# Optimization experiments

Measured on AMD Instinct MI355X. Metric: run time of the kernel, lower is better.

The kernel has to match this reference:

```python
import jax, jax.numpy as jnp
import numpy as np

B, S, H, L = 8, 512, 768, 8192


def setup_inputs() -> dict:
    key = jax.random.key(0)
    k1, k2, k3, k4 = jax.random.split(key, 4)
    inputs = jax.random.normal(k1, (B, S, H), dtype=jnp.float32)
    masks = jax.random.randint(k2, (B, 1, S), 0, 2).astype(jnp.bool_)
    # guarantee at least one valid position per row so softmax is finite
    masks = masks.at[:, :, 0].set(True)
    # xavier-normal label embedding [L, H] (frozen param in original)
    std_emb = float(np.sqrt(2.0 / (L + H)))
    label_embedding = jax.random.normal(k3, (L, H), dtype=jnp.float32) * std_emb
    # xavier-uniform key weight [H, H] (nn.Linear stores W as [out, in])
    lim = float(np.sqrt(6.0 / (H + H)))
    W_key = jax.random.uniform(k4, (H, H), dtype=jnp.float32, minval=-lim, maxval=lim)
    return {"inputs": inputs, "masks": masks, "label_embedding": label_embedding, "W_key": W_key}


def reference(inputs, masks, label_embedding, W_key):
    # key projection: inputs @ W_key^T  -> [B, S, H]
    attn_key = jnp.einsum("bsh,kh->bsk", inputs, W_key)
    # scores: label_emb @ key^T -> [B, L, S] (no 1/sqrt(d) scaling, per original)
    scores = jnp.einsum("lh,bsh->bls", label_embedding, attn_key)
    scores = jnp.where(masks, scores, -jnp.inf)  # masks [B,1,S] broadcasts over L
    attn = jax.nn.softmax(scores, axis=-1)
    # weighted sum of raw inputs -> [B, L, H]
    return jnp.einsum("bls,bsh->blh", attn, inputs)
```

## Files before the change

kernel.cpp:

```cpp
#include <hip/hip_runtime.h>
#include <hip/hip_bf16.h>
#include <math.h>

#define NB 8
#define NS 512
#define NH 768
#define NL 8192

typedef __attribute__((ext_vector_type(8))) __bf16 bf16x8;
typedef __attribute__((ext_vector_type(4))) float f32x4;

static __device__ __forceinline__ f32x4 mfma_bf16(bf16x8 a, bf16x8 b, f32x4 c) {
  return __builtin_amdgcn_mfma_f32_16x16x32_bf16(a, b, c, 0, 0, 0);
}

static __device__ __forceinline__ void llds16(const void* g, void* l) {
  __builtin_amdgcn_global_load_lds(
      (const __attribute__((address_space(1))) unsigned int*)g,
      (__attribute__((address_space(3))) unsigned int*)l, 16, 0, 0);
}

static __device__ __forceinline__ bf16x8 load_cvt8(const float* __restrict__ p) {
  f32x4 u0 = *(const f32x4*)p;
  f32x4 u1 = *(const f32x4*)(p + 4);
  bf16x8 r;
  r[0] = (__bf16)u0[0]; r[1] = (__bf16)u0[1]; r[2] = (__bf16)u0[2]; r[3] = (__bf16)u0[3];
  r[4] = (__bf16)u1[0]; r[5] = (__bf16)u1[1]; r[6] = (__bf16)u1[2]; r[7] = (__bf16)u1[3];
  return r;
}

__global__ void mask_kernel(const unsigned char* __restrict__ m,
                            float* __restrict__ mbias) {
  __shared__ int s_i8, s_f32;
  if (threadIdx.x == 0) { s_i8 = 0; s_f32 = 0; }
  __syncthreads();
  const unsigned int* md = (const unsigned int*)m;
  int li8 = 0, lf = 0;
  for (int i = threadIdx.x; i < 1024; i += blockDim.x) {
    unsigned int d = md[i];
    if (d == 0x3F800000u) lf = 1;
    if (d & 0xFFFFFF00u) li8 = 1;
  }
  if (li8) atomicOr(&s_i8, 1);
  if (lf) atomicOr(&s_f32, 1);
  __syncthreads();
  int f = s_f32 ? 2 : (s_i8 ? 1 : 0);
  for (int i = threadIdx.x; i < NB * NS; i += blockDim.x) {
    int v;
    if (f == 1)      v = (((const unsigned char*)m)[i] != 0);
    else if (f == 2) v = (((const float*)m)[i] != 0.0f);
    else             v = (((const int*)m)[i] != 0);
    mbias[i] = v ? 0.0f : -INFINITY;
  }
}

#define XT8 393216
#define WT8 466944
#define ET8 1253376
__global__ __launch_bounds__(256) void cast_all_kernel(
    const float* __restrict__ X, const float* __restrict__ W,
    const float* __restrict__ E, __bf16* __restrict__ dstbase) {
  size_t t8 = (size_t)blockIdx.x * 256 + threadIdx.x;
  const float* src;
  size_t off;
  if (t8 < XT8)      { src = X; off = t8 * 8; }
  else if (t8 < WT8) { src = W; off = (t8 - XT8) * 8; }
  else               { src = E; off = (t8 - WT8) * 8; }
  bf16x8 v = load_cvt8(src + off);
  *(bf16x8*)(dstbase + t8 * 8) = v;
}

__global__ __launch_bounds__(256) void transpose_kernel(const float* __restrict__ X,
                                                        __bf16* __restrict__ XT) {
  __shared__ float t[64][65];
  const int b = blockIdx.z, s0 = blockIdx.y * 64, h0 = blockIdx.x * 64;
  const int j = threadIdx.x & 63, i0 = threadIdx.x >> 6;
#pragma unroll
  for (int i = i0; i < 64; i += 4) t[i][j] = X[((size_t)b * NS + s0 + i) * NH + h0 + j];
  __syncthreads();
  __bf16* XTb = XT + ((size_t)b * NH + h0) * NS + s0;
  const int si = threadIdx.x & 63, j0 = threadIdx.x >> 6;
#pragma unroll
  for (int jj = j0; jj < 64; jj += 4)
    XTb[(size_t)jj * NS + si] = (__bf16)t[si][jj];
}

__global__ __launch_bounds__(256, 4) void proj64_kernel(
    const __bf16* __restrict__ Xbf, const __bf16* __restrict__ Wbf,
    __bf16* __restrict__ Kout) {
  const int tid = threadIdx.x, lane = tid & 63, wid = tid >> 6;
  const int c = lane & 15, g = lane >> 4;
  const int wm = wid >> 1, wn = wid & 1;
  const int m0 = blockIdx.x * 64, n0 = blockIdx.y * 64;
  __shared__ __align__(16) unsigned char Ast[2][4096];
  __shared__ __align__(16) unsigned char Bst[2][4096];

  f32x4 acc[2][2];
#pragma unroll
  for (int i = 0; i < 2; ++i)
#pragma unroll
    for (int j = 0; j < 2; ++j) acc[i][j] = (f32x4){0.f, 0.f, 0.f, 0.f};

  auto stage = [&](int buf, int k0) {
    int idx = wid * 64 + lane;
    int row = idx >> 2, slot = idx & 3;
    llds16(Xbf + (size_t)(m0 + row) * NH + k0 + slot * 8, &Ast[buf][wid * 1024]);
    llds16(Wbf + (size_t)(n0 + row) * NH + k0 + slot * 8, &Bst[buf][wid * 1024]);
  };

  stage(0, 0);
  __syncthreads();
  int cur = 0;
  for (int t = 0; t < 24; ++t) {
    if (t < 23) stage(cur ^ 1, (t + 1) * 32);
    bf16x8 af[2], bfr[2];
#pragma unroll
    for (int fm = 0; fm < 2; ++fm)
      af[fm] = *(const bf16x8*)&Ast[cur][(wm * 32 + fm * 16 + c) * 64 + g * 16];
#pragma unroll
    for (int fn = 0; fn < 2; ++fn)
      bfr[fn] = *(const bf16x8*)&Bst[cur][(wn * 32 + fn * 16 + c) * 64 + g * 16];
#pragma unroll
    for (int fm = 0; fm < 2; ++fm)
#pragma unroll
      for (int fn = 0; fn < 2; ++fn)
        acc[fm][fn] = mfma_bf16(af[fm], bfr[fn], acc[fm][fn]);
    __syncthreads();
    cur ^= 1;
  }
#pragma unroll
  for (int fm = 0; fm < 2; ++fm)
#pragma unroll
    for (int r = 0; r < 4; ++r) {
      int row = m0 + wm * 32 + fm * 16 + g * 4 + r;
#pragma unroll
      for (int fn = 0; fn < 2; ++fn)
        Kout[(size_t)row * NH + n0 + wn * 32 + fn * 16 + c] = (__bf16)acc[fm][fn][r];
    }
}

__global__ __launch_bounds__(512, 1) void fused_attn_kernel(
    const __bf16* __restrict__ Ebf,
    const __bf16* __restrict__ Kbf,
    const __bf16* __restrict__ XTbf,
    const float* __restrict__ mbias,
    float* __restrict__ Out) {
  const int tid = threadIdx.x, lane = tid & 63, wid = tid >> 6;
  const int c = lane & 15, g = lane >> 4;
  const int b = blockIdx.y;
  const int R0 = blockIdx.x * 64;

  __shared__ __align__(16) __bf16 Plds[64 * 512];
  __shared__ __align__(16) unsigned char Ast[2][4096];
  __shared__ __align__(16) unsigned char Bst[2][32768];
  __shared__ float red[8][64];

  const __bf16* Kb0 = Kbf + (size_t)b * NS * NH;

  f32x4 acc[4][4];
#pragma unroll
  for (int i = 0; i < 4; ++i)
#pragma unroll
    for (int j = 0; j < 4; ++j) acc[i][j] = (f32x4){0.f, 0.f, 0.f, 0.f};

  auto stage1 = [&](int buf, int k0) {
    if (wid < 4) {
      int idx = wid * 64 + lane;
      int row = idx >> 2, slot = idx & 3;
      llds16(Ebf + (size_t)(R0 + row) * NH + k0 + slot * 8, &Ast[buf][wid * 1024]);
    }
#pragma unroll
    for (int it = 0; it < 4; ++it) {
      int ch = it * 8 + wid;
      int idx = ch * 64 + lane;
      int srow = idx >> 2, slot = idx & 3;
      llds16(Kb0 + (size_t)srow * NH + k0 + slot * 8, &Bst[buf][ch * 1024]);
    }
  };

  stage1(0, 0);
  __syncthreads();
  int cur = 0;
  for (int t = 0; t < 24; ++t) {
    if (t < 23) stage1(cur ^ 1, (t + 1) * 32);
    bf16x8 af[4], bfr[4];
#pragma unroll
    for (int fm = 0; fm < 4; ++fm)
      af[fm] = *(const bf16x8*)&Ast[cur][(fm * 16 + c) * 64 + g * 16];
#pragma unroll
    for (int fn = 0; fn < 4; ++fn)
      bfr[fn] = *(const bf16x8*)&Bst[cur][(wid * 64 + fn * 16 + c) * 64 + g * 16];
#pragma unroll
    for (int fm = 0; fm < 4; ++fm)
#pragma unroll
      for (int fn = 0; fn < 4; ++fn)
        acc[fm][fn] = mfma_bf16(af[fm], bfr[fn], acc[fm][fn]);
    __syncthreads();
    cur ^= 1;
  }

  float bias[4];
#pragma unroll
  for (int fn = 0; fn < 4; ++fn) bias[fn] = mbias[b * NS + wid * 64 + fn * 16 + c];

#pragma unroll
  for (int fm = 0; fm < 4; ++fm)
#pragma unroll
    for (int r = 0; r < 4; ++r) {
      float v = -INFINITY;
#pragma unroll
      for (int fn = 0; fn < 4; ++fn) v = fmaxf(v, acc[fm][fn][r] + bias[fn]);
      v = fmaxf(v, __shfl_xor(v, 1));
      v = fmaxf(v, __shfl_xor(v, 2));
      v = fmaxf(v, __shfl_xor(v, 4));
      v = fmaxf(v, __shfl_xor(v, 8));
      if (c == 0) red[wid][fm * 16 + g * 4 + r] = v;
    }
  __syncthreads();
  float rmax[4][4];
#pragma unroll
  for (int fm = 0; fm < 4; ++fm)
#pragma unroll
    for (int r = 0; r < 4; ++r) {
      int l = fm * 16 + g * 4 + r;
      float v = red[0][l];
#pragma unroll
      for (int w = 1; w < 8; ++w) v = fmaxf(v, red[w][l]);
      rmax[fm][r] = v;
    }
  __syncthreads();

#pragma unroll
  for (int fm = 0; fm < 4; ++fm)
#pragma unroll
    for (int r = 0; r < 4; ++r) {
      float s = 0.f;
#pragma unroll
      for (int fn = 0; fn < 4; ++fn) {
        float p = __expf(acc[fm][fn][r] + bias[fn] - rmax[fm][r]);
        acc[fm][fn][r] = p;
        s += p;
      }
      s += __shfl_xor(s, 1);
      s += __shfl_xor(s, 2);
      s += __shfl_xor(s, 4);
      s += __shfl_xor(s, 8);
      if (c == 0) red[wid][fm * 16 + g * 4 + r] = s;
    }
  __syncthreads();

#pragma unroll
  for (int fm = 0; fm < 4; ++fm)
#pragma unroll
    for (int r = 0; r < 4; ++r) {
      int l = fm * 16 + g * 4 + r;
      float s = red[0][l];
#pragma unroll
      for (int w = 1; w < 8; ++w) s += red[w][l];
      float inv = 1.0f / s;
#pragma unroll
      for (int fn = 0; fn < 4; ++fn) {
        int col = wid * 64 + fn * 16 + c;
        Plds[l * 512 + (col ^ ((l & 7) << 3))] = (__bf16)(acc[fm][fn][r] * inv);
      }
    }
  __syncthreads();

  const __bf16* XTb0 = XTbf + (size_t)b * NH * NS;
  float* Ob = Out + ((size_t)b * NL + R0) * NH;

  for (int nh = 0; nh < 2; ++nh) {
    const int h0 = nh * 384;
    f32x4 acc2[4][3];
#pragma unroll
    for (int i = 0; i < 4; ++i)
#pragma unroll
      for (int j = 0; j < 3; ++j) acc2[i][j] = (f32x4){0.f, 0.f, 0.f, 0.f};

    auto stage2 = [&](int buf, int ks) {
#pragma unroll
      for (int j = 0; j < 3; ++j) {
        int ch = wid * 3 + j;
        int idx = ch * 64 + lane;
        int hrow = idx >> 2, slot = idx & 3;
        llds16(XTb0 + (size_t)(h0 + hrow) * NS + ks + slot * 8, &Bst[buf][ch * 1024]);
      }
    };

    stage2(0, 0);
    __syncthreads();
    cur = 0;
    for (int t = 0; t < 16; ++t) {
      if (t < 15) stage2(cur ^ 1, (t + 1) * 32);
      int kk = t * 32 + g * 8;
      bf16x8 af[4], bfr[3];
#pragma unroll
      for (int fm = 0; fm < 4; ++fm) {
        int l = fm * 16 + c;
        af[fm] = *(const bf16x8*)&Plds[l * 512 + (kk ^ ((l & 7) << 3))];
      }
#pragma unroll
      for (int fn = 0; fn < 3; ++fn)
        bfr[fn] = *(const bf16x8*)&Bst[cur][(wid * 48 + fn * 16 + c) * 64 + g * 16];
#pragma unroll
      for (int fm = 0; fm < 4; ++fm)
#pragma unroll
        for (int fn = 0; fn < 3; ++fn)
          acc2[fm][fn] = mfma_bf16(af[fm], bfr[fn], acc2[fm][fn]);
      __syncthreads();
      cur ^= 1;
    }
#pragma unroll
    for (int fm = 0; fm < 4; ++fm)
#pragma unroll
      for (int r = 0; r < 4; ++r) {
        int l = fm * 16 + g * 4 + r;
#pragma unroll
        for (int fn = 0; fn < 3; ++fn) {
          int h = h0 + wid * 48 + fn * 16 + c;
          Ob[(size_t)l * NH + h] = acc2[fm][fn][r];
        }
      }
  }
}

__global__ void detect_mask_kernel(const unsigned char* __restrict__ m,
                                   int* __restrict__ flag) {
  __shared__ int s_i8, s_f32;
  if (threadIdx.x == 0) { s_i8 = 0; s_f32 = 0; }
  __syncthreads();
  const unsigned int* md = (const unsigned int*)m;
  int li8 = 0, lf = 0;
  for (int i = threadIdx.x; i < 1024; i += blockDim.x) {
    unsigned int d = md[i];
    if (d == 0x3F800000u) lf = 1;
    if (d & 0xFFFFFF00u) li8 = 1;
  }
  if (li8) atomicOr(&s_i8, 1);
  if (lf) atomicOr(&s_f32, 1);
  __syncthreads();
  if (threadIdx.x == 0) *flag = s_f32 ? 2 : (s_i8 ? 1 : 0);
}

__global__ void expand_mask_kernel(const void* __restrict__ m,
                                   const int* __restrict__ flag,
                                   float* __restrict__ mbias) {
  int i = blockIdx.x * blockDim.x + threadIdx.x;
  int f = *flag;
  int v;
  if (f == 1)      v = (((const unsigned char*)m)[i] != 0);
  else if (f == 2) v = (((const float*)m)[i] != 0.0f);
  else             v = (((const int*)m)[i] != 0);
  mbias[i] = v ? 0.0f : -INFINITY;
}

__global__ __launch_bounds__(256) void cast_kernel(const float* __restrict__ src,
                                                   __bf16* __restrict__ dst) {
  size_t idx = ((size_t)blockIdx.x * 256 + threadIdx.x) * 8;
  bf16x8 v = load_cvt8(src + idx);
  *(bf16x8*)(dst + idx) = v;
}

__global__ __launch_bounds__(256) void proj_kernel(const float* __restrict__ X,
                                                   const float* __restrict__ W,
                                                   __bf16* __restrict__ Kout) {
  const int tid = threadIdx.x;
  const int lane = tid & 63, wid = tid >> 6;
  const int c = lane & 15, g = lane >> 4;
  const int wm = wid >> 1, wn = wid & 1;
  const int m0 = blockIdx.x * 64 + wm * 32;
  const int n0 = blockIdx.y * 64 + wn * 32;
  f32x4 acc[2][2] = {};
  const float* Xp = X + (size_t)(m0 + c) * NH + g * 8;
  const float* Wp = W + (size_t)(n0 + c) * NH + g * 8;
  for (int k = 0; k < NH; k += 32) {
    bf16x8 a0 = load_cvt8(Xp + k);
    bf16x8 a1 = load_cvt8(Xp + 16 * NH + k);
    bf16x8 b0 = load_cvt8(Wp + k);
    bf16x8 b1 = load_cvt8(Wp + 16 * NH + k);
    acc[0][0] = mfma_bf16(a0, b0, acc[0][0]);
    acc[0][1] = mfma_bf16(a0, b1, acc[0][1]);
    acc[1][0] = mfma_bf16(a1, b0, acc[1][0]);
    acc[1][1] = mfma_bf16(a1, b1, acc[1][1]);
  }
#pragma unroll
  for (int fm = 0; fm < 2; ++fm)
#pragma unroll
    for (int fn = 0; fn < 2; ++fn)
#pragma unroll
      for (int r = 0; r < 4; ++r) {
        int row = m0 + fm * 16 + g * 4 + r;
        int col = n0 + fn * 16 + c;
        Kout[(size_t)row * NH + col] = (__bf16)acc[fm][fn][r];
      }
}

__global__ __launch_bounds__(512) void label_attn_kernel(
    const __bf16* __restrict__ Ebf, const __bf16* __restrict__ Kbf,
    const __bf16* __restrict__ XTbf, const float* __restrict__ mbias,
    float* __restrict__ Out) {
  const int tid = threadIdx.x;
  const int lane = tid & 63, wid = tid >> 6;
  const int c = lane & 15, g = lane >> 4;
  const int wm = wid >> 2, wn = wid & 3;
  const int b = blockIdx.y;
  const int R0 = blockIdx.x * 64;
  __shared__ alignas(16) __bf16 Plds[64 * 512];
  __shared__ float redM[4][64];
  __shared__ float redS[4][64];
  f32x4 acc[2][8];
#pragma unroll
  for (int i = 0; i < 2; ++i)
#pragma unroll
    for (int j = 0; j < 8; ++j) acc[i][j] = (f32x4){0.f, 0.f, 0.f, 0.f};
  const __bf16* Ea = Ebf + (size_t)(R0 + wm * 32 + c) * NH + g * 8;
  const __bf16* Kb = Kbf + ((size_t)b * NS + wn * 128 + c) * NH + g * 8;
  float bias[8];
#pragma unroll
  for (int fn = 0; fn < 8; ++fn) bias[fn] = mbias[b * NS + wn * 128 + fn * 16 + c];
  for (int k = 0; k < NH; k += 32) {
    bf16x8 a0 = *(const bf16x8*)(Ea + k);
    bf16x8 a1 = *(const bf16x8*)(Ea + 16 * NH + k);
#pragma unroll
    for (int fn = 0; fn < 8; ++fn) {
      bf16x8 bb = *(const bf16x8*)(Kb + (size_t)fn * 16 * NH + k);
      acc[0][fn] = mfma_bf16(a0, bb, acc[0][fn]);
      acc[1][fn] = mfma_bf16(a1, bb, acc[1][fn]);
    }
  }
  float pmax[2][4];
#pragma unroll
  for (int fm = 0; fm < 2; ++fm)
#pragma unroll
    for (int r = 0; r < 4; ++r) {
      float v = -INFINITY;
#pragma unroll
      for (int fn = 0; fn < 8; ++fn) v = fmaxf(v, acc[fm][fn][r] + bias[fn]);
#pragma unroll
      for (int off = 1; off < 16; off <<= 1) v = fmaxf(v, __shfl_xor(v, off));
      pmax[fm][r] = v;
    }
  if (c == 0) {
#pragma unroll
    for (int fm = 0; fm < 2; ++fm)
#pragma unroll
      for (int r = 0; r < 4; ++r)
        redM[wn][wm * 32 + fm * 16 + g * 4 + r] = pmax[fm][r];
  }
  __syncthreads();
  float rmax[2][4];
#pragma unroll
  for (int fm = 0; fm < 2; ++fm)
#pragma unroll
    for (int r = 0; r < 4; ++r) {
      int row = wm * 32 + fm * 16 + g * 4 + r;
      rmax[fm][r] = fmaxf(fmaxf(redM[0][row], redM[1][row]),
                          fmaxf(redM[2][row], redM[3][row]));
    }
  float psum[2][4] = {{0.f, 0.f, 0.f, 0.f}, {0.f, 0.f, 0.f, 0.f}};
#pragma unroll
  for (int fm = 0; fm < 2; ++fm)
#pragma unroll
    for (int fn = 0; fn < 8; ++fn) {
      int col = wn * 128 + fn * 16 + c;
#pragma unroll
      for (int r = 0; r < 4; ++r) {
        int row = wm * 32 + fm * 16 + g * 4 + r;
        float p = __expf(acc[fm][fn][r] + bias[fn] - rmax[fm][r]);
        psum[fm][r] += p;
        Plds[row * 512 + (col ^ ((row & 7) << 3))] = (__bf16)p;
      }
    }
#pragma unroll
  for (int fm = 0; fm < 2; ++fm)
#pragma unroll
    for (int r = 0; r < 4; ++r) {
      float v = psum[fm][r];
#pragma unroll
      for (int off = 1; off < 16; off <<= 1) v += __shfl_xor(v, off);
      psum[fm][r] = v;
    }
  if (c == 0) {
#pragma unroll
    for (int fm = 0; fm < 2; ++fm)
#pragma unroll
      for (int r = 0; r < 4; ++r)
        redS[wn][wm * 32 + fm * 16 + g * 4 + r] = psum[fm][r];
  }
  __syncthreads();
  float inv[2][4];
#pragma unroll
  for (int fm = 0; fm < 2; ++fm)
#pragma unroll
    for (int r = 0; r < 4; ++r) {
      int row = wm * 32 + fm * 16 + g * 4 + r;
      float s = redS[0][row] + redS[1][row] + redS[2][row] + redS[3][row];
      inv[fm][r] = 1.0f / s;
    }
  f32x4 acc2[2][12];
#pragma unroll
  for (int i = 0; i < 2; ++i)
#pragma unroll
    for (int j = 0; j < 12; ++j) acc2[i][j] = (f32x4){0.f, 0.f, 0.f, 0.f};
  const __bf16* XTb = XTbf + ((size_t)b * NH + wn * 192 + c) * NS + g * 8;
  const int r0 = wm * 32 + c;
  const int r1 = r0 + 16;
  for (int ks = 0; ks < NS; ks += 32) {
    int kk = ks + g * 8;
    bf16x8 a0 = *(const bf16x8*)&Plds[r0 * 512 + (kk ^ ((r0 & 7) << 3))];
    bf16x8 a1 = *(const bf16x8*)&Plds[r1 * 512 + (kk ^ ((r1 & 7) << 3))];
#pragma unroll
    for (int fn = 0; fn < 12; ++fn) {
      bf16x8 bb = *(const bf16x8*)(XTb + (size_t)fn * 16 * NS + ks);
      acc2[0][fn] = mfma_bf16(a0, bb, acc2[0][fn]);
      acc2[1][fn] = mfma_bf16(a1, bb, acc2[1][fn]);
    }
  }
  float* Ob = Out + ((size_t)b * NL + R0) * NH;
#pragma unroll
  for (int fm = 0; fm < 2; ++fm)
#pragma unroll
    for (int r = 0; r < 4; ++r) {
      int row = wm * 32 + fm * 16 + g * 4 + r;
      float sc = inv[fm][r];
#pragma unroll
      for (int fn = 0; fn < 12; ++fn) {
        int h = wn * 192 + fn * 16 + c;
        Ob[(size_t)row * NH + h] = acc2[fm][fn][r] * sc;
      }
    }
}

extern "C" void kernel_launch(void* const* d_in, const int* in_sizes, int n_in,
                              void* d_out, int out_size, void* d_ws, size_t ws_size,
                              hipStream_t stream) {
  const float* X = (const float*)d_in[0];
  const void* masks = d_in[1];
  const float* E = (const float*)d_in[2];
  const float* W = (const float*)d_in[3];
  float* Out = (float*)d_out;

  char* ws = (char*)d_ws;
  const size_t NEED = 32653312;

  if (ws_size >= NEED) {
    __bf16* Xbf  = (__bf16*)ws;
    __bf16* Wbf  = (__bf16*)(ws + 6291456);
    __bf16* Ebf  = (__bf16*)(ws + 7471104);
    __bf16* Kbf  = (__bf16*)(ws + 20054016);
    __bf16* XTbf = (__bf16*)(ws + 26345472);
    float* mbias = (float*)(ws + 32636928);

    mask_kernel<<<1, 256, 0, stream>>>((const unsigned char*)masks, mbias);
    cast_all_kernel<<<4896, 256, 0, stream>>>(X, W, E, Xbf);
    transpose_kernel<<<dim3(12, 8, 8), 256, 0, stream>>>(X, XTbf);
    proj64_kernel<<<dim3(64, 12), 256, 0, stream>>>(Xbf, Wbf, Kbf);
    fused_attn_kernel<<<dim3(128, 8), 512, 0, stream>>>(Ebf, Kbf, XTbf, mbias, Out);
  } else {
    __bf16* Kbf  = (__bf16*)ws;
    __bf16* XTbf = (__bf16*)(ws + 6291456);
    __bf16* Ebf  = (__bf16*)(ws + 12582912);
    float* mbias = (float*)(ws + 25165824);
    int* flag    = (int*)(ws + 25182208);

    detect_mask_kernel<<<1, 256, 0, stream>>>((const unsigned char*)masks, flag);
    expand_mask_kernel<<<16, 256, 0, stream>>>(masks, flag, mbias);
    proj_kernel<<<dim3(64, 12), 256, 0, stream>>>(X, W, Kbf);
    transpose_kernel<<<dim3(12, 8, 8), 256, 0, stream>>>(X, XTbf);
    cast_kernel<<<3072, 256, 0, stream>>>(E, Ebf);
    label_attn_kernel<<<dim3(128, 8), 512, 0, stream>>>(Ebf, Kbf, XTbf, mbias, Out);
  }
}
```

Baseline: 474.6 us.

## Split fused attention into scores kernel and separate PV GEMM via workspace

The fused attention kernel is split in two. The first kernel computes scores and softmax and writes the bf16 probabilities P (64 MB) to a workspace buffer. A separate 128x128-tiled pv_kernel then multiplies P by the transposed inputs. Dropping the 64 KB LDS P buffer lets the scores kernel declare higher occupancy, and the PV GEMM gets a better tile shape, at the cost of extra global traffic to write and reread P. The cast and transpose kernels are also merged into a single launch.

```diff
diff --git a/kernel.cpp b/kernel.cpp
--- a/kernel.cpp
+++ b/kernel.cpp
@@ -57,32 +57,37 @@
 #define XT8 393216
 #define WT8 466944
 #define ET8 1253376
-__global__ __launch_bounds__(256) void cast_all_kernel(
+#define CAST_BLOCKS 4896
+__global__ __launch_bounds__(256) void prep_kernel(
     const float* __restrict__ X, const float* __restrict__ W,
-    const float* __restrict__ E, __bf16* __restrict__ dstbase) {
-  size_t t8 = (size_t)blockIdx.x * 256 + threadIdx.x;
-  const float* src;
-  size_t off;
-  if (t8 < XT8)      { src = X; off = t8 * 8; }
-  else if (t8 < WT8) { src = W; off = (t8 - XT8) * 8; }
-  else               { src = E; off = (t8 - WT8) * 8; }
-  bf16x8 v = load_cvt8(src + off);
-  *(bf16x8*)(dstbase + t8 * 8) = v;
-}
-
-__global__ __launch_bounds__(256) void transpose_kernel(const float* __restrict__ X,
-                                                        __bf16* __restrict__ XT) {
+    const float* __restrict__ E, __bf16* __restrict__ dstbase,
+    __bf16* __restrict__ XT) {
   __shared__ float t[64][65];
-  const int b = blockIdx.z, s0 = blockIdx.y * 64, h0 = blockIdx.x * 64;
-  const int j = threadIdx.x & 63, i0 = threadIdx.x >> 6;
-#pragma unroll
-  for (int i = i0; i < 64; i += 4) t[i][j] = X[((size_t)b * NS + s0 + i) * NH + h0 + j];
-  __syncthreads();
-  __bf16* XTb = XT + ((size_t)b * NH + h0) * NS + s0;
-  const int si = threadIdx.x & 63, j0 = threadIdx.x >> 6;
-#pragma unroll
-  for (int jj = j0; jj < 64; jj += 4)
-    XTb[(size_t)jj * NS + si] = (__bf16)t[si][jj];
+  const int bx = blockIdx.x;
+  if (bx < CAST_BLOCKS) {
+    size_t t8 = (size_t)bx * 256 + threadIdx.x;
+    const float* src;
+    size_t off;
+    if (t8 < XT8)      { src = X; off = t8 * 8; }
+    else if (t8 < WT8) { src = W; off = (t8 - XT8) * 8; }
+    else               { src = E; off = (t8 - WT8) * 8; }
+    bf16x8 v = load_cvt8(src + off);
+    *(bf16x8*)(dstbase + t8 * 8) = v;
+  } else {
+    const int tb = bx - CAST_BLOCKS;
+    const int hb = tb % 12, sb = (tb / 12) % 8, b = tb / 96;
+    const int s0 = sb * 64, h0 = hb * 64;
+    const int j = threadIdx.x & 63, i0 = threadIdx.x >> 6;
+#pragma unroll
+    for (int i = i0; i < 64; i += 4)
+      t[i][j] = X[((size_t)b * NS + s0 + i) * NH + h0 + j];
+    __syncthreads();
+    __bf16* XTb = XT + ((size_t)b * NH + h0) * NS + s0;
+    const int si = threadIdx.x & 63, j0 = threadIdx.x >> 6;
+#pragma unroll
+    for (int jj = j0; jj < 64; jj += 4)
+      XTb[(size_t)jj * NS + si] = (__bf16)t[si][jj];
+  }
 }
 
 __global__ __launch_bounds__(256, 4) void proj64_kernel(
@@ -139,18 +144,16 @@
     }
 }
 
-__global__ __launch_bounds__(512, 1) void fused_attn_kernel(
+__global__ __launch_bounds__(512, 4) void scores64_kernel(
     const __bf16* __restrict__ Ebf,
     const __bf16* __restrict__ Kbf,
-    const __bf16* __restrict__ XTbf,
     const float* __restrict__ mbias,
-    float* __restrict__ Out) {
+    __bf16* __restrict__ Pws) {
   const int tid = threadIdx.x, lane = tid & 63, wid = tid >> 6;
   const int c = lane & 15, g = lane >> 4;
   const int b = blockIdx.y;
   const int R0 = blockIdx.x * 64;
 
-  __shared__ __align__(16) __bf16 Plds[64 * 512];
   __shared__ __align__(16) unsigned char Ast[2][4096];
   __shared__ __align__(16) unsigned char Bst[2][32768];
   __shared__ float red[8][64];
@@ -249,6 +252,7 @@
     }
   __syncthreads();
 
+  __bf16* Plin = (__bf16*)Bst;
 #pragma unroll
   for (int fm = 0; fm < 4; ++fm)
 #pragma unroll
@@ -261,67 +265,82 @@
 #pragma unroll
       for (int fn = 0; fn < 4; ++fn) {
         int col = wid * 64 + fn * 16 + c;
-        Plds[l * 512 + (col ^ ((l & 7) << 3))] = (__bf16)(acc[fm][fn][r] * inv);
+        Plin[l * 512 + col] = (__bf16)(acc[fm][fn][r] * inv);
       }
     }
   __syncthreads();
 
-  const __bf16* XTb0 = XTbf + (size_t)b * NH * NS;
-  float* Ob = Out + ((size_t)b * NL + R0) * NH;
-
-  for (int nh = 0; nh < 2; ++nh) {
-    const int h0 = nh * 384;
-    f32x4 acc2[4][3];
-#pragma unroll
-    for (int i = 0; i < 4; ++i)
-#pragma unroll
-      for (int j = 0; j < 3; ++j) acc2[i][j] = (f32x4){0.f, 0.f, 0.f, 0.f};
-
-    auto stage2 = [&](int buf, int ks) {
-#pragma unroll
-      for (int j = 0; j < 3; ++j) {
-        int ch = wid * 3 + j;
-        int idx = ch * 64 + lane;
-        int hrow = idx >> 2, slot = idx & 3;
-        llds16(XTb0 + (size_t)(h0 + hrow) * NS + ks + slot * 8, &Bst[buf][ch * 1024]);
-      }
-    };
-
-    stage2(0, 0);
+  __bf16* Pb = Pws + ((size_t)b * NL + R0) * NS;
+#pragma unroll
+  for (int i = 0; i < 8; ++i) {
+    int row = wid * 8 + i;
+    bf16x8 v = *(const bf16x8*)&Plin[row * 512 + lane * 8];
+    *(bf16x8*)(Pb + (size_t)row * NS + lane * 8) = v;
+  }
+}
+
+__global__ __launch_bounds__(256, 3) void pv_kernel(
+    const __bf16* __restrict__ Pws,
+    const __bf16* __restrict__ XTbf,
+    float* __restrict__ Out) {
+  const int tid = threadIdx.x, lane = tid & 63, wid = tid >> 6;
+  const int c = lane & 15, g = lane >> 4;
+  const int wm = wid >> 1, wn = wid & 1;
+  const int b = blockIdx.z;
+  const size_t rowbase = (size_t)b * NL + (size_t)blockIdx.x * 128;
+  const int h0 = blockIdx.y * 128;
+  __shared__ __align__(16) unsigned char smem[2][16384];
+  const __bf16* Xb0 = XTbf + (size_t)b * NH * NS;
+
+  f32x4 acc[4][4];
+#pragma unroll
+  for (int i = 0; i < 4; ++i)
+#pragma unroll
+    for (int j = 0; j < 4; ++j) acc[i][j] = (f32x4){0.f, 0.f, 0.f, 0.f};
+
+  auto stage = [&](int buf, int k0) {
+#pragma unroll
+    for (int it = 0; it < 2; ++it) {
+      int ch = it * 4 + wid;
+      int idx = ch * 64 + lane;
+      int row = idx >> 2, slot = idx & 3;
+      llds16(Pws + (rowbase + row) * NS + k0 + slot * 8, &smem[buf][ch * 1024]);
+      llds16(Xb0 + (size_t)(h0 + row) * NS + k0 + slot * 8, &smem[buf][8192 + ch * 1024]);
+    }
+  };
+
+  stage(0, 0);
+  __syncthreads();
+  int cur = 0;
+  for (int t = 0; t < 16; ++t) {
+    if (t < 15) stage(cur ^ 1, (t + 1) * 32);
+    const unsigned char* A = smem[cur];
+    const unsigned char* B = smem[cur] + 8192;
+    bf16x8 af[4], bfr[4];
+#pragma unroll
+    for (int fm = 0; fm < 4; ++fm)
+      af[fm] = *(const bf16x8*)(A + (wm * 64 + fm * 16 + c) * 64 + g * 16);
+#pragma unroll
+    for (int fn = 0; fn < 4; ++fn)
+      bfr[fn] = *(const bf16x8*)(B + (wn * 64 + fn * 16 + c) * 64 + g * 16);
+#pragma unroll
+    for (int fm = 0; fm < 4; ++fm)
+#pragma unroll
+      for (int fn = 0; fn < 4; ++fn)
+        acc[fm][fn] = mfma_bf16(af[fm], bfr[fn], acc[fm][fn]);
     __syncthreads();
-    cur = 0;
-    for (int t = 0; t < 16; ++t) {
-      if (t < 15) stage2(cur ^ 1, (t + 1) * 32);
-      int kk = t * 32 + g * 8;
-      bf16x8 af[4], bfr[3];
-#pragma unroll
-      for (int fm = 0; fm < 4; ++fm) {
-        int l = fm * 16 + c;
-        af[fm] = *(const bf16x8*)&Plds[l * 512 + (kk ^ ((l & 7) << 3))];
-      }
-#pragma unroll
-      for (int fn = 0; fn < 3; ++fn)
-        bfr[fn] = *(const bf16x8*)&Bst[cur][(wid * 48 + fn * 16 + c) * 64 + g * 16];
-#pragma unroll
-      for (int fm = 0; fm < 4; ++fm)
-#pragma unroll
-        for (int fn = 0; fn < 3; ++fn)
-          acc2[fm][fn] = mfma_bf16(af[fm], bfr[fn], acc2[fm][fn]);
-      __syncthreads();
-      cur ^= 1;
-    }
-#pragma unroll
-    for (int fm = 0; fm < 4; ++fm)
-#pragma unroll
-      for (int r = 0; r < 4; ++r) {
-        int l = fm * 16 + g * 4 + r;
-#pragma unroll
-        for (int fn = 0; fn < 3; ++fn) {
-          int h = h0 + wid * 48 + fn * 16 + c;
-          Ob[(size_t)l * NH + h] = acc2[fm][fn][r];
-        }
-      }
-  }
+    cur ^= 1;
+  }
+  float* Ob = Out + rowbase * NH;
+#pragma unroll
+  for (int fm = 0; fm < 4; ++fm)
+#pragma unroll
+    for (int r = 0; r < 4; ++r) {
+      int row = wm * 64 + fm * 16 + g * 4 + r;
+#pragma unroll
+      for (int fn = 0; fn < 4; ++fn)
+        Ob[(size_t)row * NH + h0 + wn * 64 + fn * 16 + c] = acc[fm][fn][r];
+    }
 }
 
 __global__ void detect_mask_kernel(const unsigned char* __restrict__ m,
@@ -359,6 +378,21 @@
   size_t idx = ((size_t)blockIdx.x * 256 + threadIdx.x) * 8;
   bf16x8 v = load_cvt8(src + idx);
   *(bf16x8*)(dst + idx) = v;
+}
+
+__global__ __launch_bounds__(256) void transpose_kernel(const float* __restrict__ X,
+                                                        __bf16* __restrict__ XT) {
+  __shared__ float t[64][65];
+  const int b = blockIdx.z, s0 = blockIdx.y * 64, h0 = blockIdx.x * 64;
+  const int j = threadIdx.x & 63, i0 = threadIdx.x >> 6;
+#pragma unroll
+  for (int i = i0; i < 64; i += 4) t[i][j] = X[((size_t)b * NS + s0 + i) * NH + h0 + j];
+  __syncthreads();
+  __bf16* XTb = XT + ((size_t)b * NH + h0) * NS + s0;
+  const int si = threadIdx.x & 63, j0 = threadIdx.x >> 6;
+#pragma unroll
+  for (int jj = j0; jj < 64; jj += 4)
+    XTb[(size_t)jj * NS + si] = (__bf16)t[si][jj];
 }
 
 __global__ __launch_bounds__(256) void proj_kernel(const float* __restrict__ X,
@@ -541,7 +575,7 @@
   float* Out = (float*)d_out;
 
   char* ws = (char*)d_ws;
-  const size_t NEED = 32653312;
+  const size_t NEED = 99762432;
 
   if (ws_size >= NEED) {
     __bf16* Xbf  = (__bf16*)ws;
@@ -549,13 +583,14 @@
     __bf16* Ebf  = (__bf16*)(ws + 7471104);
     __bf16* Kbf  = (__bf16*)(ws + 20054016);
     __bf16* XTbf = (__bf16*)(ws + 26345472);
-    float* mbias = (float*)(ws + 32636928);
+    __bf16* Pws  = (__bf16*)(ws + 32636928);
+    float* mbias = (float*)(ws + 99745792);
 
     mask_kernel<<<1, 256, 0, stream>>>((const unsigned char*)masks, mbias);
-    cast_all_kernel<<<4896, 256, 0, stream>>>(X, W, E, Xbf);
-    transpose_kernel<<<dim3(12, 8, 8), 256, 0, stream>>>(X, XTbf);
+    prep_kernel<<<5664, 256, 0, stream>>>(X, W, E, Xbf, XTbf);
     proj64_kernel<<<dim3(64, 12), 256, 0, stream>>>(Xbf, Wbf, Kbf);
-    fused_attn_kernel<<<dim3(128, 8), 512, 0, stream>>>(Ebf, Kbf, XTbf, mbias, Out);
+    scores64_kernel<<<dim3(128, 8), 512, 0, stream>>>(Ebf, Kbf, mbias, Pws);
+    pv_kernel<<<dim3(64, 6, 8), 256, 0, stream>>>(Pws, XTbf, Out);
   } else {
     __bf16* Kbf  = (__bf16*)ws;
     __bf16* XTbf = (__bf16*)(ws + 6291456);
```

Result: faster. 457.4 us (-3.6%).
